# Optimization experiments

Hardware: AMD Instinct MI355X
Metric: run time of the kernel (lower is better)

Reference implementation:

```python
import jax, jax.numpy as jnp
import numpy as np

N = 50000        # nodes
E = 800000       # edges (before self-loops)
IN = 128         # in_channels
HID = 256        # hidden_channels
HEADS = 8
C = HID // HEADS # per-head channels = 32
NC = 64          # num_classes
L = 3            # num_layers - 1 hidden GATConv layers


def setup_inputs() -> dict:
    key = jax.random.key(0)
    ks = jax.random.split(key, 12)
    x = jax.random.normal(ks[0], (N, IN), dtype=jnp.float32)
    edge_index = jax.random.randint(ks[1], (2, E), 0, N, dtype=jnp.int64)
    s = 0.05
    W0 = jax.random.normal(ks[2], (IN, HID), jnp.float32) * s
    b0 = jnp.zeros((HID,), jnp.float32)
    Wc = jax.random.normal(ks[3], (L, HID, HID), jnp.float32) * s
    a_src_c = jax.random.normal(ks[4], (L, HEADS, C), jnp.float32) * s
    a_dst_c = jax.random.normal(ks[5], (L, HEADS, C), jnp.float32) * s
    bc = jnp.zeros((L, HID), jnp.float32)
    Wl = jax.random.normal(ks[6], (HID, NC), jnp.float32) * s
    a_src_l = jax.random.normal(ks[7], (1, NC), jnp.float32) * s
    a_dst_l = jax.random.normal(ks[8], (1, NC), jnp.float32) * s
    bl = jnp.zeros((NC,), jnp.float32)
    return {"x": x, "edge_index": edge_index, "W0": W0, "b0": b0,
            "Wc": Wc, "a_src_c": a_src_c, "a_dst_c": a_dst_c, "bc": bc,
            "Wl": Wl, "a_src_l": a_src_l, "a_dst_l": a_dst_l, "bl": bl}


def gat_layer(h_in, W, a_s, a_d, b, src, dst, n, heads, c, concat):
    # PyG GATConv: h = x W -> [n, heads, c]
    h = (h_in @ W).reshape(n, heads, c)
    alpha_s = jnp.einsum('nhc,hc->nh', h, a_s)  # [n, heads]
    alpha_d = jnp.einsum('nhc,hc->nh', h, a_d)
    e = jax.nn.leaky_relu(alpha_s[src] + alpha_d[dst], 0.2)  # [E', heads]
    # scatter-softmax over incoming edges of each destination node
    m = jax.ops.segment_max(e, dst, num_segments=n)
    ex = jnp.exp(e - m[dst])
    den = jax.ops.segment_sum(ex, dst, num_segments=n)
    att = ex / (den[dst] + 1e-16)                            # [E', heads]
    out = jax.ops.segment_sum(h[src] * att[:, :, None], dst, num_segments=n)
    out = out.reshape(n, heads * c) if concat else out.mean(axis=1)
    return out + b


def reference(x, edge_index, W0, b0, Wc, a_src_c, a_dst_c, bc, Wl, a_src_l, a_dst_l, bl):
    n = x.shape[0]
    loops = jnp.arange(n, dtype=edge_index.dtype)
    src = jnp.concatenate([edge_index[0], loops])  # GATConv adds self-loops
    dst = jnp.concatenate([edge_index[1], loops])
    h = x @ W0 + b0                                 # node_embed
    xs = [h]
    for l in range(Wc.shape[0]):
        h = gat_layer(h, Wc[l], a_src_c[l], a_dst_c[l], bc[l], src, dst, n, HEADS, C, True)
        h = jax.nn.relu(h)                          # dropout p=0 (eval)
        xs.append(h)
    out = gat_layer(h, Wl, a_src_l, a_dst_l, bl, src, dst, n, 1, NC, False)
    xs.append(out)
    return jnp.concatenate(xs, axis=-1)             # JumpingKnowledge 'cat'
```

## Files before the change

### kernel.cpp

```cpp
#include <hip/hip_runtime.h>

typedef __attribute__((ext_vector_type(8))) short short8v;
typedef __attribute__((ext_vector_type(4))) float f32x4;

#define IN_CH 128
#define HID   256
#define HEADS 8
#define NCLS  64
#define LDO   1088
#define LDOU  2176

__device__ __forceinline__ unsigned short f2b(float f) {
    unsigned u = __float_as_uint(f);
    u += 0x7FFFu + ((u >> 16) & 1u);
    return (unsigned short)(u >> 16);
}
__device__ __forceinline__ float b2f(unsigned short s) {
    return __uint_as_float(((unsigned)s) << 16);
}

__global__ void detect64(const int* __restrict__ ei, int* __restrict__ flag, int E) {
    __shared__ int nz;
    if (threadIdx.x == 0) nz = 0;
    __syncthreads();
    int v = ei[2 * threadIdx.x + 1];
    if (v != 0) atomicAdd(&nz, 1);
    __syncthreads();
    if (threadIdx.x == 0) flag[0] = (nz == 0) ? 1 : 0;
}

__global__ void hist_k(const int* __restrict__ ei, const int* __restrict__ flag,
                       int* __restrict__ deg, int E) {
    int i = blockIdx.x * 256 + threadIdx.x;
    if (i >= E) return;
    int is64 = flag[0];
    int dst = is64 ? ei[2 * (E + i)] : ei[E + i];
    atomicAdd(&deg[dst], 1);
}

__global__ void scan_k(const int* __restrict__ deg, int* __restrict__ rowptr, int N) {
    __shared__ int sums[1024];
    int t = threadIdx.x;
    int chunk = (N + 1023) >> 10;
    int beg = t * chunk;
    int end = beg + chunk; if (end > N) end = N;
    if (beg > N) beg = N;
    int s = 0;
    for (int i = beg; i < end; ++i) s += deg[i];
    sums[t] = s;
    __syncthreads();
    for (int o = 1; o < 1024; o <<= 1) {
        int v = (t >= o) ? sums[t - o] : 0;
        __syncthreads();
        sums[t] += v;
        __syncthreads();
    }
    int run = (t == 0) ? 0 : sums[t - 1];
    for (int i = beg; i < end; ++i) { rowptr[i] = run; run += deg[i]; }
    if (t == 1023) rowptr[N] = sums[1023];
}

__global__ void fill_k(const int* __restrict__ ei, const int* __restrict__ flag,
                       const int* __restrict__ rowptr, int* __restrict__ cnt,
                       int* __restrict__ colb, int E) {
    int i = blockIdx.x * 256 + threadIdx.x;
    if (i >= E) return;
    int is64 = flag[0];
    int src, dst;
    if (is64) { src = ei[2 * i]; dst = ei[2 * (E + i)]; }
    else      { src = ei[i];     dst = ei[E + i]; }
    int pos = rowptr[dst] + atomicAdd(&cnt[dst], 1);
    colb[pos] = src;
}

__global__ void convw_all(const float* __restrict__ W0, const float* __restrict__ Wc,
                          const float* __restrict__ Wl,
                          unsigned short* __restrict__ W0T, unsigned short* __restrict__ WcT,
                          unsigned short* __restrict__ WlT) {
    int i = blockIdx.x * 256 + threadIdx.x;
    if (i < 32768) {
        int k = i >> 8, n = i & 255;
        W0T[n * 128 + k] = f2b(W0[i]);
    } else if (i < 229376) {
        int j = i - 32768;
        int l = j >> 16, r = j & 65535;
        int k = r >> 8, n = r & 255;
        WcT[l * 65536 + n * 256 + k] = f2b(Wc[j]);
    } else if (i < 245760) {
        int j = i - 229376;
        int k = j >> 6, n = j & 63;
        WlT[n * 256 + k] = f2b(Wl[j]);
    }
}

__global__ void convx(const float* __restrict__ x, unsigned short* __restrict__ xb, int n) {
    int idx = blockIdx.x * 256 + threadIdx.x;
    int node = idx >> 5, c = (idx & 31) * 4;
    if (node >= n) return;
    float4 v = *(const float4*)(x + (size_t)node * IN_CH + c);
    ushort4 w;
    w.x = f2b(v.x); w.y = f2b(v.y); w.z = f2b(v.z); w.w = f2b(v.w);
    *(ushort4*)(xb + (size_t)node * LDOU + c) = w;
}

#define GBM 128
#define GBN 64
#define GBK 64
#define GLD 72

template<int AF32, int MODE>
__global__ __launch_bounds__(256) void gemm_bf16(
    const void* __restrict__ Av, int lda,
    const unsigned short* __restrict__ BT,
    int M, int K,
    float* __restrict__ outF, const float* __restrict__ bias,
    unsigned short* __restrict__ outB, int ostride)
{
    __shared__ unsigned short Asm[GBM][GLD];
    __shared__ unsigned short Bsm[GBN][GLD];
    const int t = threadIdx.x;
    const int wid = t >> 6, lane = t & 63;
    const int m0 = blockIdx.x * GBM;
    const int n0 = blockIdx.y * GBN;
    const int wm = (wid >> 1) * 64;
    const int wn = (wid & 1) * 32;

    f32x4 acc[4][2];
#pragma unroll
    for (int i = 0; i < 4; ++i)
#pragma unroll
        for (int j = 0; j < 2; ++j) acc[i][j] = (f32x4)0.f;

    const int rA = lane & 15;
    const int kk8 = (lane >> 4) * 8;

    for (int k0 = 0; k0 < K; k0 += GBK) {
        __syncthreads();
        if (AF32) {
            const float* A = (const float*)Av;
#pragma unroll
            for (int p = 0; p < 8; ++p) {
                int idx = p * 256 + t;
                int row = idx >> 4, c4 = (idx & 15) * 4;
                int grow = m0 + row;
                float4 v = make_float4(0.f, 0.f, 0.f, 0.f);
                if (grow < M) v = *(const float4*)(A + (size_t)grow * lda + k0 + c4);
                ushort4 w;
                w.x = f2b(v.x); w.y = f2b(v.y); w.z = f2b(v.z); w.w = f2b(v.w);
                *(ushort4*)&Asm[row][c4] = w;
            }
        } else {
            const unsigned short* A = (const unsigned short*)Av;
#pragma unroll
            for (int p = 0; p < 4; ++p) {
                int idx = p * 256 + t;
                int row = idx >> 3, ch = (idx & 7) * 8;
                int grow = m0 + row;
                int4 v = make_int4(0, 0, 0, 0);
                if (grow < M) v = *(const int4*)(A + (size_t)grow * lda + k0 + ch);
                *(int4*)&Asm[row][ch] = v;
            }
        }
#pragma unroll
        for (int p = 0; p < 2; ++p) {
            int idx = p * 256 + t;
            int row = idx >> 3, ch = (idx & 7) * 8;
            int4 v = *(const int4*)(BT + (size_t)(n0 + row) * K + k0 + ch);
            *(int4*)&Bsm[row][ch] = v;
        }
        __syncthreads();
#pragma unroll
        for (int s = 0; s < 2; ++s) {
            short8v af[4], bfv[2];
#pragma unroll
            for (int i = 0; i < 4; ++i) af[i] = *(const short8v*)&Asm[wm + i * 16 + rA][s * 32 + kk8];
#pragma unroll
            for (int j = 0; j < 2; ++j) bfv[j] = *(const short8v*)&Bsm[wn + j * 16 + rA][s * 32 + kk8];
#pragma unroll
            for (int i = 0; i < 4; ++i)
#pragma unroll
                for (int j = 0; j < 2; ++j)
                    acc[i][j] = __builtin_amdgcn_mfma_f32_16x16x32_bf16(af[i], bfv[j], acc[i][j], 0, 0, 0);
        }
    }

    const int cr = (lane >> 4) * 4;
    const int cc = lane & 15;
#pragma unroll
    for (int i = 0; i < 4; ++i)
#pragma unroll
        for (int j = 0; j < 2; ++j)
#pragma unroll
            for (int r = 0; r < 4; ++r) {
                int row = m0 + wm + i * 16 + cr + r;
                int col = n0 + wn + j * 16 + cc;
                if (row >= M) continue;
                float v = acc[i][j][r];
                if (MODE == 0) {
                    outB[(size_t)row * ostride + col] = f2b(v);
                } else {
                    v += bias[col];
                    outF[(size_t)row * LDO + col] = v;
                    if (MODE == 2) outB[(size_t)row * ostride + col] = f2b(v);
                }
            }
}

__global__ void alpha8(const unsigned short* __restrict__ tb, int tstride,
                       const float* __restrict__ as_, const float* __restrict__ ad_,
                       float* __restrict__ aS, float* __restrict__ aD, int n) {
    int wid = threadIdx.x >> 6, lane = threadIdx.x & 63;
    int node = blockIdx.x * 4 + wid;
    if (node >= n) return;
    int c = lane * 4;
    ushort4 hv = *(const ushort4*)(tb + (size_t)node * tstride + c);
    float4 av = *(const float4*)(as_ + c);
    float4 dv = *(const float4*)(ad_ + c);
    float h0 = b2f(hv.x), h1 = b2f(hv.y), h2 = b2f(hv.z), h3 = b2f(hv.w);
    float s = h0 * av.x + h1 * av.y + h2 * av.z + h3 * av.w;
    float d = h0 * dv.x + h1 * dv.y + h2 * dv.z + h3 * dv.w;
    s += __shfl_xor(s, 1); s += __shfl_xor(s, 2); s += __shfl_xor(s, 4);
    d += __shfl_xor(d, 1); d += __shfl_xor(d, 2); d += __shfl_xor(d, 4);
    if ((lane & 7) == 0) {
        aS[node * HEADS + (lane >> 3)] = s;
        aD[node * HEADS + (lane >> 3)] = d;
    }
}

__global__ void alpha1(const unsigned short* __restrict__ tb64, int tstride,
                       const float* __restrict__ as_, const float* __restrict__ ad_,
                       float* __restrict__ aS, float* __restrict__ aD, int n) {
    int wid = threadIdx.x >> 6, lane = threadIdx.x & 63;
    int node = blockIdx.x * 4 + wid;
    if (node >= n) return;
    float v = b2f(tb64[(size_t)node * tstride + lane]);
    float s = v * as_[lane], d = v * ad_[lane];
#pragma unroll
    for (int o = 1; o < 64; o <<= 1) { s += __shfl_xor(s, o); d += __shfl_xor(d, o); }
    if (lane == 0) { aS[node] = s; aD[node] = d; }
}

__global__ void agg8(const int* __restrict__ rowptr, const int* __restrict__ colb,
                     const float* __restrict__ aS, const float* __restrict__ aD,
                     const unsigned short* __restrict__ tb, int tstride,
                     const float* __restrict__ bias,
                     float* __restrict__ outp, unsigned short* __restrict__ outb,
                     int n, int dorelu) {
    int wid = threadIdx.x >> 6, lane = threadIdx.x & 63;
    int node = blockIdx.x * 4 + wid;
    if (node >= n) return;
    int c = lane * 4, head = lane >> 3;
    float aDv = aD[node * HEADS + head];
    float xs = aS[node * HEADS + head] + aDv;
    xs = xs > 0.f ? xs : 0.2f * xs;
    float wS = __expf(xs);
    float den = wS + 1e-16f;
    ushort4 hv0 = *(const ushort4*)(tb + (size_t)node * tstride + c);
    float a0 = wS * b2f(hv0.x), a1 = wS * b2f(hv0.y);
    float a2 = wS * b2f(hv0.z), a3 = wS * b2f(hv0.w);
    int s0 = rowptr[node], s1 = rowptr[node + 1];
#pragma unroll 2
    for (int e = s0; e < s1; ++e) {
        int src = colb[e];
        float xx = aS[src * HEADS + head] + aDv;
        xx = xx > 0.f ? xx : 0.2f * xx;
        float w = __expf(xx);
        den += w;
        ushort4 hv = *(const ushort4*)(tb + (size_t)src * tstride + c);
        a0 += w * b2f(hv.x); a1 += w * b2f(hv.y);
        a2 += w * b2f(hv.z); a3 += w * b2f(hv.w);
    }
    float inv = 1.f / den;
    float4 bv = *(const float4*)(bias + c);
    float o0 = a0 * inv + bv.x, o1 = a1 * inv + bv.y;
    float o2 = a2 * inv + bv.z, o3 = a3 * inv + bv.w;
    if (dorelu) {
        o0 = fmaxf(o0, 0.f); o1 = fmaxf(o1, 0.f);
        o2 = fmaxf(o2, 0.f); o3 = fmaxf(o3, 0.f);
    }
    *(float4*)(outp + (size_t)node * LDO + c) = make_float4(o0, o1, o2, o3);
    ushort4 ob;
    ob.x = f2b(o0); ob.y = f2b(o1); ob.z = f2b(o2); ob.w = f2b(o3);
    *(ushort4*)(outb + (size_t)node * LDOU + c) = ob;
}

__global__ void agg1(const int* __restrict__ rowptr, const int* __restrict__ colb,
                     const float* __restrict__ aS, const float* __restrict__ aD,
                     const unsigned short* __restrict__ tb64, int tstride,
                     const float* __restrict__ bl,
                     float* __restrict__ outp, int n) {
    int wid = threadIdx.x >> 6, lane = threadIdx.x & 63;
    int node = blockIdx.x * 4 + wid;
    if (node >= n) return;
    float aDv = aD[node];
    float xs = aS[node] + aDv;
    xs = xs > 0.f ? xs : 0.2f * xs;
    float wS = __expf(xs);
    float den = wS + 1e-16f;
    float acc = wS * b2f(tb64[(size_t)node * tstride + lane]);
    int s0 = rowptr[node], s1 = rowptr[node + 1];
#pragma unroll 2
    for (int e = s0; e < s1; ++e) {
        int src = colb[e];
        float xx = aS[src] + aDv;
        xx = xx > 0.f ? xx : 0.2f * xx;
        float w = __expf(xx);
        den += w;
        acc += w * b2f(tb64[(size_t)src * tstride + lane]);
    }
    outp[(size_t)node * LDO + 1024 + lane] = acc / den + bl[lane];
}

extern "C" void kernel_launch(void* const* d_in, const int* in_sizes, int n_in,
                              void* d_out, int out_size, void* d_ws, size_t ws_size,
                              hipStream_t stream) {
    const float* x   = (const float*)d_in[0];
    const int*   ei  = (const int*)d_in[1];
    const float* W0  = (const float*)d_in[2];
    const float* b0  = (const float*)d_in[3];
    const float* Wc  = (const float*)d_in[4];
    const float* asc = (const float*)d_in[5];
    const float* adc = (const float*)d_in[6];
    const float* bc  = (const float*)d_in[7];
    const float* Wl  = (const float*)d_in[8];
    const float* asl = (const float*)d_in[9];
    const float* adl = (const float*)d_in[10];
    const float* bl  = (const float*)d_in[11];
    float* out = (float*)d_out;
    unsigned short* outU = (unsigned short*)d_out;

    const int N = in_sizes[0] / IN_CH;
    const int E = in_sizes[1] / 2;

    char* ws = (char*)d_ws;
    size_t off = 0;
    auto take = [&](size_t bytes) -> void* {
        void* p = ws + off;
        off += (bytes + 255) & ~(size_t)255;
        return p;
    };
    unsigned short* WbT = (unsigned short*)take((size_t)245760 * 2);
    float* aS   = (float*)take((size_t)N * HEADS * 4);
    float* aD   = (float*)take((size_t)N * HEADS * 4);
    int* deg    = (int*)take((size_t)N * 4);
    int* cnt    = (int*)take((size_t)N * 4);
    int* rowptr = (int*)take((size_t)(N + 1) * 4);
    int* colb   = (int*)take((size_t)E * 4);
    int* flag   = (int*)take(256);

    unsigned short* W0T = WbT;
    unsigned short* WcT = WbT + 32768;
    unsigned short* WlT = WbT + 32768 + 3 * 65536;

    hipMemsetAsync(deg, 0, (size_t)N * 4, stream);
    hipMemsetAsync(cnt, 0, (size_t)N * 4, stream);

    detect64<<<1, 256, 0, stream>>>(ei, flag, E);
    convw_all<<<960, 256, 0, stream>>>(W0, Wc, Wl, W0T, WcT, WlT);
    convx<<<(N * 32 + 255) / 256, 256, 0, stream>>>(x, outU + 512, N);

    hist_k<<<(E + 255) / 256, 256, 0, stream>>>(ei, flag, deg, E);
    scan_k<<<1, 1024, 0, stream>>>(deg, rowptr, N);
    fill_k<<<(E + 255) / 256, 256, 0, stream>>>(ei, flag, rowptr, cnt, colb, E);

    const int gmx = (N + GBM - 1) / GBM;
    const int nwb = (N + 3) / 4;

    gemm_bf16<0, 2><<<dim3(gmx, 4), 256, 0, stream>>>(outU + 512, LDOU, W0T, N, 128,
                                                      out, b0, outU + 768, LDOU);

    const unsigned short* Ab[3] = { outU + 768, outU + 1024, outU + 1792 };
    unsigned short* tbs[3]      = { outU + 1792, outU + 1536, outU };
    unsigned short* hb[3]       = { outU + 1024, outU + 1792, outU + 256 };
    for (int l = 0; l < 3; ++l) {
        gemm_bf16<0, 0><<<dim3(gmx, 4), 256, 0, stream>>>(Ab[l], LDOU, WcT + l * 65536, N, 256,
                                                          nullptr, nullptr, tbs[l], LDOU);
        alpha8<<<nwb, 256, 0, stream>>>(tbs[l], LDOU, asc + l * 256, adc + l * 256, aS, aD, N);
        agg8<<<nwb, 256, 0, stream>>>(rowptr, colb, aS, aD, tbs[l], LDOU, bc + l * 256,
                                      out + 256 * (l + 1), hb[l], N, 1);
    }

    gemm_bf16<0, 0><<<dim3(gmx, 1), 256, 0, stream>>>(outU + 256, LDOU, WlT, N, 256,
                                                      nullptr, nullptr, outU, LDOU);
    alpha1<<<nwb, 256, 0, stream>>>(outU, LDOU, asl, adl, aS, aD, N);
    agg1<<<nwb, 256, 0, stream>>>(rowptr, colb, aS, aD, outU, LDOU, bl, out, N);

    gemm_bf16<1, 1><<<dim3(gmx, 4), 256, 0, stream>>>(x, IN_CH, W0T, N, 128,
                                                      out, b0, nullptr, 0);
}
```

Before: 867.4 us.

## Fuse attention logits into GEMM epilogue and split edge aggregation across two waves

Attention score dot products for the hidden GAT layers are now computed in the GEMM epilogue from the fp32 accumulators, so the separate alpha8 kernel and its re-read of the projected features are gone. The per-node aggregation kernel now gives each node two wavefronts that each take half the incoming edges and combine partial sums through shared memory. This shortens the serial edge loop per node at the cost of a block barrier and fewer nodes per block. The weight and input conversion kernels are merged into one launch, and the two memsets are merged into one, to cut launch overhead.

```diff
diff --git a/kernel.cpp b/kernel.cpp
--- a/kernel.cpp
+++ b/kernel.cpp
@@ -73,34 +73,32 @@
     colb[pos] = src;
 }
 
-__global__ void convw_all(const float* __restrict__ W0, const float* __restrict__ Wc,
-                          const float* __restrict__ Wl,
-                          unsigned short* __restrict__ W0T, unsigned short* __restrict__ WcT,
-                          unsigned short* __restrict__ WlT) {
+__global__ void prep(const float* __restrict__ W0, const float* __restrict__ Wc,
+                     const float* __restrict__ Wl, const float* __restrict__ x,
+                     unsigned short* __restrict__ W0T, unsigned short* __restrict__ WcT,
+                     unsigned short* __restrict__ WlT, unsigned short* __restrict__ xb, int n) {
     int i = blockIdx.x * 256 + threadIdx.x;
     if (i < 32768) {
-        int k = i >> 8, n = i & 255;
-        W0T[n * 128 + k] = f2b(W0[i]);
+        int k = i >> 8, c = i & 255;
+        W0T[c * 128 + k] = f2b(W0[i]);
     } else if (i < 229376) {
         int j = i - 32768;
         int l = j >> 16, r = j & 65535;
-        int k = r >> 8, n = r & 255;
-        WcT[l * 65536 + n * 256 + k] = f2b(Wc[j]);
+        int k = r >> 8, c = r & 255;
+        WcT[l * 65536 + c * 256 + k] = f2b(Wc[j]);
     } else if (i < 245760) {
         int j = i - 229376;
-        int k = j >> 6, n = j & 63;
-        WlT[n * 256 + k] = f2b(Wl[j]);
-    }
-}
-
-__global__ void convx(const float* __restrict__ x, unsigned short* __restrict__ xb, int n) {
-    int idx = blockIdx.x * 256 + threadIdx.x;
-    int node = idx >> 5, c = (idx & 31) * 4;
-    if (node >= n) return;
-    float4 v = *(const float4*)(x + (size_t)node * IN_CH + c);
-    ushort4 w;
-    w.x = f2b(v.x); w.y = f2b(v.y); w.z = f2b(v.z); w.w = f2b(v.w);
-    *(ushort4*)(xb + (size_t)node * LDOU + c) = w;
+        int k = j >> 6, c = j & 63;
+        WlT[c * 256 + k] = f2b(Wl[j]);
+    } else {
+        int idx = i - 245760;
+        int node = idx >> 5, c = (idx & 31) * 4;
+        if (node >= n) return;
+        float4 v = *(const float4*)(x + (size_t)node * IN_CH + c);
+        ushort4 w;
+        w.x = f2b(v.x); w.y = f2b(v.y); w.z = f2b(v.z); w.w = f2b(v.w);
+        *(ushort4*)(xb + (size_t)node * LDOU + c) = w;
+    }
 }
 
 #define GBM 128
@@ -108,13 +106,15 @@
 #define GBK 64
 #define GLD 72
 
-template<int AF32, int MODE>
+template<int AF32, int MODE, int ALPHA>
 __global__ __launch_bounds__(256) void gemm_bf16(
     const void* __restrict__ Av, int lda,
     const unsigned short* __restrict__ BT,
     int M, int K,
     float* __restrict__ outF, const float* __restrict__ bias,
-    unsigned short* __restrict__ outB, int ostride)
+    unsigned short* __restrict__ outB, int ostride,
+    const float* __restrict__ as_, const float* __restrict__ ad_,
+    float* __restrict__ aSo, float* __restrict__ aDo)
 {
     __shared__ unsigned short Asm[GBM][GLD];
     __shared__ unsigned short Bsm[GBN][GLD];
@@ -204,26 +204,29 @@
                     if (MODE == 2) outB[(size_t)row * ostride + col] = f2b(v);
                 }
             }
-}
-
-__global__ void alpha8(const unsigned short* __restrict__ tb, int tstride,
-                       const float* __restrict__ as_, const float* __restrict__ ad_,
-                       float* __restrict__ aS, float* __restrict__ aD, int n) {
-    int wid = threadIdx.x >> 6, lane = threadIdx.x & 63;
-    int node = blockIdx.x * 4 + wid;
-    if (node >= n) return;
-    int c = lane * 4;
-    ushort4 hv = *(const ushort4*)(tb + (size_t)node * tstride + c);
-    float4 av = *(const float4*)(as_ + c);
-    float4 dv = *(const float4*)(ad_ + c);
-    float h0 = b2f(hv.x), h1 = b2f(hv.y), h2 = b2f(hv.z), h3 = b2f(hv.w);
-    float s = h0 * av.x + h1 * av.y + h2 * av.z + h3 * av.w;
-    float d = h0 * dv.x + h1 * dv.y + h2 * dv.z + h3 * dv.w;
-    s += __shfl_xor(s, 1); s += __shfl_xor(s, 2); s += __shfl_xor(s, 4);
-    d += __shfl_xor(d, 1); d += __shfl_xor(d, 2); d += __shfl_xor(d, 4);
-    if ((lane & 7) == 0) {
-        aS[node * HEADS + (lane >> 3)] = s;
-        aD[node * HEADS + (lane >> 3)] = d;
+
+    if (ALPHA && MODE == 0) {
+        const int head = (n0 + wn) >> 5;
+        const float asv0 = as_[n0 + wn + cc], asv1 = as_[n0 + wn + 16 + cc];
+        const float adv0 = ad_[n0 + wn + cc], adv1 = ad_[n0 + wn + 16 + cc];
+#pragma unroll
+        for (int i = 0; i < 4; ++i)
+#pragma unroll
+            for (int r = 0; r < 4; ++r) {
+                float ps = acc[i][0][r] * asv0 + acc[i][1][r] * asv1;
+                float pd = acc[i][0][r] * adv0 + acc[i][1][r] * adv1;
+                ps += __shfl_xor(ps, 1); ps += __shfl_xor(ps, 2);
+                ps += __shfl_xor(ps, 4); ps += __shfl_xor(ps, 8);
+                pd += __shfl_xor(pd, 1); pd += __shfl_xor(pd, 2);
+                pd += __shfl_xor(pd, 4); pd += __shfl_xor(pd, 8);
+                if ((lane & 15) == 0) {
+                    int row = m0 + wm + i * 16 + cr + r;
+                    if (row < M) {
+                        aSo[row * HEADS + head] = ps;
+                        aDo[row * HEADS + head] = pd;
+                    }
+                }
+            }
     }
 }
 
@@ -246,42 +249,64 @@
                      const float* __restrict__ bias,
                      float* __restrict__ outp, unsigned short* __restrict__ outb,
                      int n, int dorelu) {
-    int wid = threadIdx.x >> 6, lane = threadIdx.x & 63;
-    int node = blockIdx.x * 4 + wid;
-    if (node >= n) return;
+    __shared__ float comb[2][64][5];
+    int t = threadIdx.x;
+    int wid = t >> 6, lane = t & 63;
+    int p = wid >> 1, q = wid & 1;
+    int node = blockIdx.x * 2 + p;
+    bool valid = node < n;
     int c = lane * 4, head = lane >> 3;
-    float aDv = aD[node * HEADS + head];
-    float xs = aS[node * HEADS + head] + aDv;
-    xs = xs > 0.f ? xs : 0.2f * xs;
-    float wS = __expf(xs);
-    float den = wS + 1e-16f;
-    ushort4 hv0 = *(const ushort4*)(tb + (size_t)node * tstride + c);
-    float a0 = wS * b2f(hv0.x), a1 = wS * b2f(hv0.y);
-    float a2 = wS * b2f(hv0.z), a3 = wS * b2f(hv0.w);
-    int s0 = rowptr[node], s1 = rowptr[node + 1];
-#pragma unroll 2
-    for (int e = s0; e < s1; ++e) {
-        int src = colb[e];
-        float xx = aS[src * HEADS + head] + aDv;
-        xx = xx > 0.f ? xx : 0.2f * xx;
-        float w = __expf(xx);
-        den += w;
-        ushort4 hv = *(const ushort4*)(tb + (size_t)src * tstride + c);
-        a0 += w * b2f(hv.x); a1 += w * b2f(hv.y);
-        a2 += w * b2f(hv.z); a3 += w * b2f(hv.w);
-    }
-    float inv = 1.f / den;
-    float4 bv = *(const float4*)(bias + c);
-    float o0 = a0 * inv + bv.x, o1 = a1 * inv + bv.y;
-    float o2 = a2 * inv + bv.z, o3 = a3 * inv + bv.w;
-    if (dorelu) {
-        o0 = fmaxf(o0, 0.f); o1 = fmaxf(o1, 0.f);
-        o2 = fmaxf(o2, 0.f); o3 = fmaxf(o3, 0.f);
-    }
-    *(float4*)(outp + (size_t)node * LDO + c) = make_float4(o0, o1, o2, o3);
-    ushort4 ob;
-    ob.x = f2b(o0); ob.y = f2b(o1); ob.z = f2b(o2); ob.w = f2b(o3);
-    *(ushort4*)(outb + (size_t)node * LDOU + c) = ob;
+    float a0 = 0.f, a1 = 0.f, a2 = 0.f, a3 = 0.f, den = 0.f;
+    float aDv = 0.f;
+    if (valid) {
+        aDv = aD[node * HEADS + head];
+        int s0 = rowptr[node], s1 = rowptr[node + 1];
+        int mid = (s0 + s1 + 1) >> 1;
+        int eb = q ? mid : s0;
+        int ee = q ? s1 : mid;
+        if (q == 0) {
+            float xs = aS[node * HEADS + head] + aDv;
+            xs = xs > 0.f ? xs : 0.2f * xs;
+            float wS = __expf(xs);
+            den = wS + 1e-16f;
+            ushort4 hv0 = *(const ushort4*)(tb + (size_t)node * tstride + c);
+            a0 = wS * b2f(hv0.x); a1 = wS * b2f(hv0.y);
+            a2 = wS * b2f(hv0.z); a3 = wS * b2f(hv0.w);
+        }
+        for (int e = eb; e < ee; ++e) {
+            int src = colb[e];
+            float xx = aS[src * HEADS + head] + aDv;
+            xx = xx > 0.f ? xx : 0.2f * xx;
+            float w = __expf(xx);
+            den += w;
+            ushort4 hv = *(const ushort4*)(tb + (size_t)src * tstride + c);
+            a0 += w * b2f(hv.x); a1 += w * b2f(hv.y);
+            a2 += w * b2f(hv.z); a3 += w * b2f(hv.w);
+        }
+    }
+    if (q == 1) {
+        comb[p][lane][0] = a0; comb[p][lane][1] = a1;
+        comb[p][lane][2] = a2; comb[p][lane][3] = a3;
+        comb[p][lane][4] = den;
+    }
+    __syncthreads();
+    if (valid && q == 0) {
+        a0 += comb[p][lane][0]; a1 += comb[p][lane][1];
+        a2 += comb[p][lane][2]; a3 += comb[p][lane][3];
+        den += comb[p][lane][4];
+        float inv = 1.f / den;
+        float4 bv = *(const float4*)(bias + c);
+        float o0 = a0 * inv + bv.x, o1 = a1 * inv + bv.y;
+        float o2 = a2 * inv + bv.z, o3 = a3 * inv + bv.w;
+        if (dorelu) {
+            o0 = fmaxf(o0, 0.f); o1 = fmaxf(o1, 0.f);
+            o2 = fmaxf(o2, 0.f); o3 = fmaxf(o3, 0.f);
+        }
+        *(float4*)(outp + (size_t)node * LDO + c) = make_float4(o0, o1, o2, o3);
+        ushort4 ob;
+        ob.x = f2b(o0); ob.y = f2b(o1); ob.z = f2b(o2); ob.w = f2b(o3);
+        *(ushort4*)(outb + (size_t)node * LDOU + c) = ob;
+    }
 }
 
 __global__ void agg1(const int* __restrict__ rowptr, const int* __restrict__ colb,
@@ -352,12 +377,11 @@
     unsigned short* WcT = WbT + 32768;
     unsigned short* WlT = WbT + 32768 + 3 * 65536;
 
-    hipMemsetAsync(deg, 0, (size_t)N * 4, stream);
-    hipMemsetAsync(cnt, 0, (size_t)N * 4, stream);
+    hipMemsetAsync(deg, 0, (size_t)((char*)cnt - (char*)deg) + (size_t)N * 4, stream);
 
     detect64<<<1, 256, 0, stream>>>(ei, flag, E);
-    convw_all<<<960, 256, 0, stream>>>(W0, Wc, Wl, W0T, WcT, WlT);
-    convx<<<(N * 32 + 255) / 256, 256, 0, stream>>>(x, outU + 512, N);
+    prep<<<(245760 + N * 32 + 255) / 256, 256, 0, stream>>>(W0, Wc, Wl, x, W0T, WcT, WlT,
+                                                            outU + 512, N);
 
     hist_k<<<(E + 255) / 256, 256, 0, stream>>>(ei, flag, deg, E);
     scan_k<<<1, 1024, 0, stream>>>(deg, rowptr, N);
@@ -365,26 +389,30 @@
 
     const int gmx = (N + GBM - 1) / GBM;
     const int nwb = (N + 3) / 4;
-
-    gemm_bf16<0, 2><<<dim3(gmx, 4), 256, 0, stream>>>(outU + 512, LDOU, W0T, N, 128,
-                                                      out, b0, outU + 768, LDOU);
+    const int nb2 = (N + 1) / 2;
+
+    gemm_bf16<0, 2, 0><<<dim3(gmx, 4), 256, 0, stream>>>(outU + 512, LDOU, W0T, N, 128,
+                                                         out, b0, outU + 768, LDOU,
+                                                         nullptr, nullptr, nullptr, nullptr);
 
     const unsigned short* Ab[3] = { outU + 768, outU + 1024, outU + 1792 };
     unsigned short* tbs[3]      = { outU + 1792, outU + 1536, outU };
     unsigned short* hb[3]       = { outU + 1024, outU + 1792, outU + 256 };
     for (int l = 0; l < 3; ++l) {
-        gemm_bf16<0, 0><<<dim3(gmx, 4), 256, 0, stream>>>(Ab[l], LDOU, WcT + l * 65536, N, 256,
-                                                          nullptr, nullptr, tbs[l], LDOU);
-        alpha8<<<nwb, 256, 0, stream>>>(tbs[l], LDOU, asc + l * 256, adc + l * 256, aS, aD, N);
-        agg8<<<nwb, 256, 0, stream>>>(rowptr, colb, aS, aD, tbs[l], LDOU, bc + l * 256,
+        gemm_bf16<0, 0, 1><<<dim3(gmx, 4), 256, 0, stream>>>(Ab[l], LDOU, WcT + l * 65536, N, 256,
+                                                             nullptr, nullptr, tbs[l], LDOU,
+                                                             asc + l * 256, adc + l * 256, aS, aD);
+        agg8<<<nb2, 256, 0, stream>>>(rowptr, colb, aS, aD, tbs[l], LDOU, bc + l * 256,
                                       out + 256 * (l + 1), hb[l], N, 1);
     }
 
-    gemm_bf16<0, 0><<<dim3(gmx, 1), 256, 0, stream>>>(outU + 256, LDOU, WlT, N, 256,
-                                                      nullptr, nullptr, outU, LDOU);
+    gemm_bf16<0, 0, 0><<<dim3(gmx, 1), 256, 0, stream>>>(outU + 256, LDOU, WlT, N, 256,
+                                                         nullptr, nullptr, outU, LDOU,
+                                                         nullptr, nullptr, nullptr, nullptr);
     alpha1<<<nwb, 256, 0, stream>>>(outU, LDOU, asl, adl, aS, aD, N);
     agg1<<<nwb, 256, 0, stream>>>(rowptr, colb, aS, aD, outU, LDOU, bl, out, N);
 
-    gemm_bf16<1, 1><<<dim3(gmx, 4), 256, 0, stream>>>(x, IN_CH, W0T, N, 128,
-                                                      out, b0, nullptr, 0);
-}
+    gemm_bf16<1, 1, 0><<<dim3(gmx, 4), 256, 0, stream>>>(x, IN_CH, W0T, N, 128,
+                                                         out, b0, nullptr, 0,
+                                                         nullptr, nullptr, nullptr, nullptr);
+}
```

After: 938.5 us. 1.08x slower.
